# Kernel optimization log

Hardware: AMD Instinct MI355X
Metric: run time of the kernel (lower is better)

## Reference

```python
import jax, jax.numpy as jnp
import numpy as np
import math

D = 384  # hidden_dim; seq_len must equal D, batch must be 1 (torch broadcast constraint)
S = 384
B = 1


def grad_seq(x):
    """torch.gradient along axis 1: one-sided at edges, central in interior."""
    left = x[:, 1:2] - x[:, 0:1]
    mid = (x[:, 2:] - x[:, :-2]) * 0.5
    right = x[:, -1:] - x[:, -2:-1]
    return jnp.concatenate([left, mid, right], axis=1)


def setup_inputs() -> dict:
    key = jax.random.key(0)
    ks = jax.random.split(key, 8)
    return {
        "query_field": jax.random.normal(ks[0], (B, S, D), jnp.float32),
        "key_field": jax.random.normal(ks[1], (B, S, D), jnp.float32),
        "value_field": jax.random.normal(ks[2], (B, S, D), jnp.float32),
        "gauge_weights": jax.random.normal(ks[3], (D, D), jnp.float32) * 0.01,
        "covariant_weights": jax.random.normal(ks[4], (D, D), jnp.float32) * 0.01,
        "yang_mills_coupling": jnp.asarray(1.0, jnp.float32),
        "lag_w1": jax.random.normal(ks[5], (2 * D, D), jnp.float32) * (1.0 / math.sqrt(2 * D)),
        "lag_b1": jnp.zeros((D,), jnp.float32),
        "lag_w2": jax.random.normal(ks[6], (D, 1), jnp.float32) * (1.0 / math.sqrt(D)),
        "lag_b2": jnp.zeros((1,), jnp.float32),
    }


def reference(query_field, key_field, value_field, gauge_weights, covariant_weights,
              yang_mills_coupling, lag_w1, lag_b1, lag_w2, lag_b2):
    q, k, v = query_field, key_field, value_field

    # ---- field strength F_munu -------------------------------------------
    ga = grad_seq(q)                                   # [B,S,D]
    gb = grad_seq(k)
    # commutator: per-token dim x dim outer products
    comm = q[..., :, None] * k[..., None, :] - k[..., :, None] * q[..., None, :]  # [B,S,D,D]
    cm = comm.mean(axis=-1)                            # [B,S,D]
    # torch broadcast: [B,S,D,1]-[B,S,1,D] + [B,S,D] (left-padded to [1,B,S,D]); valid since B=1, S=D
    field_strength = ga[..., :, None] - gb[..., None, :] + cm  # [1,S,D,D]

    # ---- covariant derivatives -------------------------------------------
    cov_q = grad_seq(q) + q @ covariant_weights        # [B,S,D]
    cov_k = grad_seq(k) + k @ covariant_weights

    # ---- interaction energy (Lagrangian MLP) ------------------------------
    combined = jnp.concatenate([cov_q, cov_k], axis=-1)          # [B,S,2D]
    h = jax.nn.relu(combined @ lag_w1 + lag_b1)
    interaction_density = h @ lag_w2 + lag_b2                    # [B,S,1]
    interaction_energy = interaction_density.sum(axis=1)         # [B,1]

    # ---- gauge-invariant attention ----------------------------------------
    logits = jnp.einsum('bqd,bkd->bqk', cov_q, cov_k) / math.sqrt(D)  # [B,S,S]
    gauge_corr = (field_strength @ gauge_weights).sum(axis=-1)        # [B,S,D]
    # torch broadcast: [B,S,S] + [B,S,D,1] -> [1,S,D,S] (valid since S=D)
    gal = logits + gauge_corr[..., None]                              # [1,S,D,S]
    attention_weights = jax.nn.softmax(gal, axis=-1)                  # [1,S,D,S]

    evolved_field = jnp.matmul(attention_weights, v)                  # [1,S,S,D]

    # ---- metrics ------------------------------------------------------------
    yang_mills_action = yang_mills_coupling * jnp.sum(field_strength ** 2, axis=(-2, -1)).sum(axis=1)  # [B]

    second = grad_seq(grad_seq(evolved_field))
    field_curvature = jnp.linalg.norm(second, axis=-1).mean(axis=1)   # [1,S]

    init_e = jnp.sum(q ** 2, axis=(-2, -1))                           # [B]
    fin_e = jnp.sum(evolved_field ** 2, axis=(-2, -1))                # [1,S]
    conservation = jnp.abs(fin_e - init_e) / (init_e + 1e-8)          # [1,S]

    row_sums = attention_weights.sum(axis=-1)
    gauge_inv = jnp.clip(1.0 - jnp.std(row_sums, ddof=1), 0.0, 1.0)

    flat = evolved_field.reshape(evolved_field.shape[0], -1)
    coherence = jnp.mean(jnp.abs(jnp.corrcoef(flat)))                 # scalar (==1 for B=1)

    topo = (field_strength.sum(axis=(-2, -1)) / (2 * math.pi)).mean(axis=1)  # [B]

    return (evolved_field, field_strength, interaction_energy, yang_mills_action,
            field_curvature, gauge_inv, conservation, coherence, topo)
```

## Files before the change

### kernel.cpp

```cpp
#include <hip/hip_runtime.h>

#define S_ 384
#define D_ 384
#define SD_ (384*384)

#define OUT_EV 0
#define OUT_FS 56623104
#define OUT_IE 113246208
#define OUT_YM 113246209
#define OUT_FC 113246210
#define OUT_GI 113246594
#define OUT_CO 113246595
#define OUT_CH 113246979
#define OUT_TP 113246980

typedef __attribute__((ext_vector_type(4))) float f32x4;

__device__ __forceinline__ float waveSum(float v){
  v += __shfl_down(v,32); v += __shfl_down(v,16); v += __shfl_down(v,8);
  v += __shfl_down(v,4);  v += __shfl_down(v,2);  v += __shfl_down(v,1);
  return v;
}
__device__ __forceinline__ float waveMax(float v){
  v = fmaxf(v,__shfl_down(v,32)); v = fmaxf(v,__shfl_down(v,16)); v = fmaxf(v,__shfl_down(v,8));
  v = fmaxf(v,__shfl_down(v,4));  v = fmaxf(v,__shfl_down(v,2));  v = fmaxf(v,__shfl_down(v,1));
  return v;
}
__device__ __forceinline__ double waveSumD(double v){
  v += __shfl_down(v,32); v += __shfl_down(v,16); v += __shfl_down(v,8);
  v += __shfl_down(v,4);  v += __shfl_down(v,2);  v += __shfl_down(v,1);
  return v;
}

__device__ __forceinline__ void writeF_block(int id, int t,
    const float* __restrict__ ga, const float* __restrict__ gb,
    const float* __restrict__ cm, float* __restrict__ outF){
  __shared__ float gbs[D_];
  __shared__ float gas[64];
  int bs = id/6, ch = id%6, i0 = ch*64;
  gbs[t] = gb[bs*D_+t];
  if (t<64) gas[t] = ga[bs*D_+i0+t];
  __syncthreads();
  const f32x4* cm4 = (const f32x4*)(cm + i0*D_);
  const f32x4* gb4 = (const f32x4*)gbs;
  f32x4* o4 = (f32x4*)(outF + ((size_t)bs*S_ + i0)*D_);
  #pragma unroll
  for (int u=0; u<16; u++){
    int f = t + u*384;
    int il = f/96;
    int j4 = f - il*96;
    f32x4 o = gas[il] - gb4[j4] + cm4[f];
    o4[f] = o;
  }
}
__device__ __forceinline__ void writeE_block(int id, int t,
    const float* __restrict__ E, float* __restrict__ outE){
  int bs = id/6, ch = id%6, i0 = ch*64;
  const f32x4* e4 = (const f32x4*)(E + i0*D_);
  f32x4* o4 = (f32x4*)(outE + ((size_t)bs*S_ + i0)*D_);
  #pragma unroll
  for (int u=0; u<16; u++){
    int f = t + u*384;
    o4[f] = e4[f];
  }
}

__global__ __launch_bounds__(384) void k1(
    const float* __restrict__ q, const float* __restrict__ k,
    const float* __restrict__ W,
    float* __restrict__ ga, float* __restrict__ gb, float* __restrict__ cm,
    float* __restrict__ pq2,
    float* __restrict__ cq, float* __restrict__ ck, float* __restrict__ ckT){
  int b = blockIdx.x, t = threadIdx.x;
  if (b < 384){
    int s = b;
    float a = q[s*D_+t], bb = k[s*D_+t];
    float sq = waveSum(a), sk = waveSum(bb), sq2 = waveSum(a*a);
    __shared__ float red[3][6];
    int wid=t>>6, lane=t&63;
    if (lane==0){ red[0][wid]=sq; red[1][wid]=sk; red[2][wid]=sq2; }
    __syncthreads();
    float qm=0,km=0,q2=0;
    #pragma unroll
    for (int w=0;w<6;w++){ qm+=red[0][w]; km+=red[1][w]; q2+=red[2][w]; }
    qm *= (1.0f/D_); km *= (1.0f/D_);
    if (t==0) pq2[s]=q2;
    int sm=(s==0)?0:s-1, sp=(s==S_-1)?S_-1:s+1;
    float sc=(s==0||s==S_-1)?1.f:0.5f;
    ga[s*D_+t] = (q[sp*D_+t]-q[sm*D_+t])*sc;
    gb[s*D_+t] = (k[sp*D_+t]-k[sm*D_+t])*sc;
    cm[s*D_+t] = a*km - bb*qm;
  } else if (b < 480){
    int s0 = (b-384)*4;
    const float* r0=q+(s0+0)*D_; const float* r1=q+(s0+1)*D_;
    const float* r2=q+(s0+2)*D_; const float* r3=q+(s0+3)*D_;
    float a0=0,a1=0,a2=0,a3=0;
    for (int e=0;e<D_;e+=4){
      float w0=W[(e+0)*D_+t], w1=W[(e+1)*D_+t], w2=W[(e+2)*D_+t], w3=W[(e+3)*D_+t];
      f32x4 x;
      x=*(const f32x4*)(r0+e); a0 += x.x*w0 + x.y*w1 + x.z*w2 + x.w*w3;
      x=*(const f32x4*)(r1+e); a1 += x.x*w0 + x.y*w1 + x.z*w2 + x.w*w3;
      x=*(const f32x4*)(r2+e); a2 += x.x*w0 + x.y*w1 + x.z*w2 + x.w*w3;
      x=*(const f32x4*)(r3+e); a3 += x.x*w0 + x.y*w1 + x.z*w2 + x.w*w3;
    }
    float acc[4]={a0,a1,a2,a3};
    #pragma unroll
    for (int r=0;r<4;r++){
      int s=s0+r;
      int sm=(s==0)?0:s-1, sp=(s==S_-1)?S_-1:s+1;
      float sc=(s==0||s==S_-1)?1.f:0.5f;
      cq[s*D_+t] = acc[r] + (q[sp*D_+t]-q[sm*D_+t])*sc;
    }
  } else {
    int s0 = (b-480)*4;
    const float* r0=k+(s0+0)*D_; const float* r1=k+(s0+1)*D_;
    const float* r2=k+(s0+2)*D_; const float* r3=k+(s0+3)*D_;
    float a0=0,a1=0,a2=0,a3=0;
    for (int e=0;e<D_;e+=4){
      float w0=W[(e+0)*D_+t], w1=W[(e+1)*D_+t], w2=W[(e+2)*D_+t], w3=W[(e+3)*D_+t];
      f32x4 x;
      x=*(const f32x4*)(r0+e); a0 += x.x*w0 + x.y*w1 + x.z*w2 + x.w*w3;
      x=*(const f32x4*)(r1+e); a1 += x.x*w0 + x.y*w1 + x.z*w2 + x.w*w3;
      x=*(const f32x4*)(r2+e); a2 += x.x*w0 + x.y*w1 + x.z*w2 + x.w*w3;
      x=*(const f32x4*)(r3+e); a3 += x.x*w0 + x.y*w1 + x.z*w2 + x.w*w3;
    }
    float acc[4]={a0,a1,a2,a3};
    float o[4];
    #pragma unroll
    for (int r=0;r<4;r++){
      int s=s0+r;
      int sm=(s==0)?0:s-1, sp=(s==S_-1)?S_-1:s+1;
      float sc=(s==0||s==S_-1)?1.f:0.5f;
      o[r] = acc[r] + (k[sp*D_+t]-k[sm*D_+t])*sc;
      ck[s*D_+t] = o[r];
    }
    f32x4 tr; tr.x=o[0]; tr.y=o[1]; tr.z=o[2]; tr.w=o[3];
    *(f32x4*)(ckT + t*D_ + s0) = tr;
  }
}

__global__ __launch_bounds__(384) void k2(
    const float* __restrict__ covq, const float* __restrict__ covk,
    const float* __restrict__ ckT, const float* __restrict__ v,
    const float* __restrict__ W1, const float* __restrict__ b1,
    const float* __restrict__ W2,
    float* __restrict__ E, float* __restrict__ pE2, float* __restrict__ pen,
    const float* __restrict__ ga, const float* __restrict__ gb,
    const float* __restrict__ cm,
    float* __restrict__ Sga, float* __restrict__ Sgb, float* __restrict__ Rcm,
    float* __restrict__ P2, float* __restrict__ Cga, float* __restrict__ Cgb,
    float* __restrict__ Ccm, float* __restrict__ outF){
  int b = blockIdx.x, t = threadIdx.x;
  if (b < 96){
    int i0 = b*4;
    __shared__ float P[4][D_];
    __shared__ float wred[4][6];
    __shared__ float wred2[4][6];
    __shared__ float sred[6];
    const float* q0=covq+(i0+0)*D_; const float* q1=covq+(i0+1)*D_;
    const float* q2=covq+(i0+2)*D_; const float* q3=covq+(i0+3)*D_;
    float l0=0,l1=0,l2=0,l3=0;
    for (int e=0;e<D_;e+=4){
      float c0=ckT[(e+0)*D_+t], c1=ckT[(e+1)*D_+t], c2=ckT[(e+2)*D_+t], c3=ckT[(e+3)*D_+t];
      f32x4 a;
      a=*(const f32x4*)(q0+e); l0 += a.x*c0 + a.y*c1 + a.z*c2 + a.w*c3;
      a=*(const f32x4*)(q1+e); l1 += a.x*c0 + a.y*c1 + a.z*c2 + a.w*c3;
      a=*(const f32x4*)(q2+e); l2 += a.x*c0 + a.y*c1 + a.z*c2 + a.w*c3;
      a=*(const f32x4*)(q3+e); l3 += a.x*c0 + a.y*c1 + a.z*c2 + a.w*c3;
    }
    const float isq = 0.05103103630798288f;
    l0*=isq; l1*=isq; l2*=isq; l3*=isq;
    float m0=waveMax(l0), m1=waveMax(l1), m2=waveMax(l2), m3=waveMax(l3);
    int wid=t>>6, lane=t&63;
    if (lane==0){ wred[0][wid]=m0; wred[1][wid]=m1; wred[2][wid]=m2; wred[3][wid]=m3; }
    __syncthreads();
    float mx0=wred[0][0], mx1=wred[1][0], mx2=wred[2][0], mx3=wred[3][0];
    for (int w=1; w<6; w++){
      mx0=fmaxf(mx0,wred[0][w]); mx1=fmaxf(mx1,wred[1][w]);
      mx2=fmaxf(mx2,wred[2][w]); mx3=fmaxf(mx3,wred[3][w]);
    }
    float e0=expf(l0-mx0), e1=expf(l1-mx1), e2=expf(l2-mx2), e3=expf(l3-mx3);
    float s0=waveSum(e0), s1=waveSum(e1), s2=waveSum(e2), s3=waveSum(e3);
    if (lane==0){ wred2[0][wid]=s0; wred2[1][wid]=s1; wred2[2][wid]=s2; wred2[3][wid]=s3; }
    __syncthreads();
    float d0=0,d1=0,d2=0,d3=0;
    for (int w=0; w<6; w++){ d0+=wred2[0][w]; d1+=wred2[1][w]; d2+=wred2[2][w]; d3+=wred2[3][w]; }
    P[0][t]=e0/d0; P[1][t]=e1/d1; P[2][t]=e2/d2; P[3][t]=e3/d3;
    __syncthreads();
    float ea0=0,ea1=0,ea2=0,ea3=0;
    for (int t2=0; t2<D_; t2+=4){
      float v0 = v[(t2+0)*D_+t];
      float v1 = v[(t2+1)*D_+t];
      float v2 = v[(t2+2)*D_+t];
      float v3 = v[(t2+3)*D_+t];
      f32x4 p;
      p=*(const f32x4*)&P[0][t2]; ea0 += p.x*v0 + p.y*v1 + p.z*v2 + p.w*v3;
      p=*(const f32x4*)&P[1][t2]; ea1 += p.x*v0 + p.y*v1 + p.z*v2 + p.w*v3;
      p=*(const f32x4*)&P[2][t2]; ea2 += p.x*v0 + p.y*v1 + p.z*v2 + p.w*v3;
      p=*(const f32x4*)&P[3][t2]; ea3 += p.x*v0 + p.y*v1 + p.z*v2 + p.w*v3;
    }
    E[(i0+0)*D_+t]=ea0; E[(i0+1)*D_+t]=ea1; E[(i0+2)*D_+t]=ea2; E[(i0+3)*D_+t]=ea3;
    float se2 = ea0*ea0+ea1*ea1+ea2*ea2+ea3*ea3;
    se2 = waveSum(se2);
    if (lane==0) sred[wid]=se2;
    __syncthreads();
    if (t==0) pE2[b] = sred[0]+sred[1]+sred[2]+sred[3]+sred[4]+sred[5];
  } else if (b < 192){
    int s0 = (b-96)*4;
    __shared__ float sred2[6];
    const float* c0=covq+(s0+0)*D_; const float* c1=covq+(s0+1)*D_;
    const float* c2=covq+(s0+2)*D_; const float* c3=covq+(s0+3)*D_;
    const float* d0=covk+(s0+0)*D_; const float* d1=covk+(s0+1)*D_;
    const float* d2=covk+(s0+2)*D_; const float* d3=covk+(s0+3)*D_;
    float h0=0,h1=0,h2=0,h3=0;
    for (int e=0; e<D_; e+=4){
      float w0=W1[(e+0)*D_+t], w1=W1[(e+1)*D_+t], w2=W1[(e+2)*D_+t], w3=W1[(e+3)*D_+t];
      f32x4 x;
      x=*(const f32x4*)(c0+e); h0 += x.x*w0 + x.y*w1 + x.z*w2 + x.w*w3;
      x=*(const f32x4*)(c1+e); h1 += x.x*w0 + x.y*w1 + x.z*w2 + x.w*w3;
      x=*(const f32x4*)(c2+e); h2 += x.x*w0 + x.y*w1 + x.z*w2 + x.w*w3;
      x=*(const f32x4*)(c3+e); h3 += x.x*w0 + x.y*w1 + x.z*w2 + x.w*w3;
    }
    for (int e=0; e<D_; e+=4){
      float w0=W1[(D_+e+0)*D_+t], w1=W1[(D_+e+1)*D_+t], w2=W1[(D_+e+2)*D_+t], w3=W1[(D_+e+3)*D_+t];
      f32x4 x;
      x=*(const f32x4*)(d0+e); h0 += x.x*w0 + x.y*w1 + x.z*w2 + x.w*w3;
      x=*(const f32x4*)(d1+e); h1 += x.x*w0 + x.y*w1 + x.z*w2 + x.w*w3;
      x=*(const f32x4*)(d2+e); h2 += x.x*w0 + x.y*w1 + x.z*w2 + x.w*w3;
      x=*(const f32x4*)(d3+e); h3 += x.x*w0 + x.y*w1 + x.z*w2 + x.w*w3;
    }
    float bb=b1[t], w2c=W2[t];
    h0=fmaxf(h0+bb,0.f); h1=fmaxf(h1+bb,0.f); h2=fmaxf(h2+bb,0.f); h3=fmaxf(h3+bb,0.f);
    float p = (h0+h1+h2+h3)*w2c;
    p = waveSum(p);
    int wid=t>>6, lane=t&63;
    if (lane==0) sred2[wid]=p;
    __syncthreads();
    if (t==0) pen[b-96] = sred2[0]+sred2[1]+sred2[2]+sred2[3]+sred2[4]+sred2[5];
  } else if (b < 576){
    int rb = b-192;
    float ra=ga[rb*D_+t], rg=gb[rb*D_+t], rc=cm[rb*D_+t];
    float ca=ga[t*D_+rb], cg=gb[t*D_+rb], cc=cm[t*D_+rb];
    float p2 = ra*ra + rg*rg + rc*rc;
    float s0=waveSum(ra), s1=waveSum(rg), s2=waveSum(rc), s3=waveSum(p2);
    float s4=waveSum(ca), s5=waveSum(cg), s6=waveSum(cc);
    __shared__ float red[7][6];
    int wid=t>>6, lane=t&63;
    if (lane==0){ red[0][wid]=s0; red[1][wid]=s1; red[2][wid]=s2; red[3][wid]=s3;
                  red[4][wid]=s4; red[5][wid]=s5; red[6][wid]=s6; }
    __syncthreads();
    if (t==0){
      float a0=0,a1=0,a2=0,a3=0,a4=0,a5=0,a6=0;
      for (int w=0;w<6;w++){ a0+=red[0][w]; a1+=red[1][w]; a2+=red[2][w]; a3+=red[3][w];
                             a4+=red[4][w]; a5+=red[5][w]; a6+=red[6][w]; }
      Sga[rb]=a0; Sgb[rb]=a1; Rcm[rb]=a2; P2[rb]=a3; Cga[rb]=a4; Cgb[rb]=a5; Ccm[rb]=a6;
    }
  } else {
    writeF_block(b-576, t, ga, gb, cm, outF);
  }
}

__global__ __launch_bounds__(384) void k3(
    const float* __restrict__ E, float* __restrict__ outE,
    const float* __restrict__ pq2,
    const float* __restrict__ Sga, const float* __restrict__ Sgb,
    const float* __restrict__ Rcm, const float* __restrict__ P2,
    const float* __restrict__ Cga, const float* __restrict__ Cgb,
    const float* __restrict__ Ccm,
    const float* __restrict__ pE2, const float* __restrict__ pen,
    const float* __restrict__ coup, const float* __restrict__ b2,
    float* __restrict__ out){
  int b = blockIdx.x, t = threadIdx.x;
  if (b == 0){
    double v[10];
    v[0]=pq2[t];
    v[1]=Sga[t]; v[2]=Sgb[t]; v[3]=Rcm[t]; v[4]=P2[t];
    v[5]=(double)Sga[t]*Sgb[t];
    v[6]=(double)Cga[t]*Rcm[t];
    v[7]=(double)Cgb[t]*Ccm[t];
    v[8]=(t<96)? (double)pE2[t] : 0.0;
    v[9]=(t<96)? (double)pen[t] : 0.0;
    __shared__ double red[10][6];
    int wid=t>>6, lane=t&63;
    #pragma unroll
    for (int i=0;i<10;i++){
      double s = waveSumD(v[i]);
      if (lane==0) red[i][wid]=s;
    }
    __syncthreads();
    double tot[10];
    #pragma unroll
    for (int i=0;i<10;i++){
      double s=0; for (int w=0;w<6;w++) s+=red[i][w];
      tot[i]=s;
    }
    double init_e=tot[0], fin_e=tot[8], en=tot[9];
    double sumF  = 384.0*(tot[1]-tot[2]+tot[3]);
    double sumF2 = 384.0*tot[4] - 2.0*tot[5] + 2.0*tot[6] - 2.0*tot[7];
    float cons = (float)(fabs(fin_e - init_e)/(init_e + 1e-8));
    out[OUT_FC + t] = 0.0f;
    out[OUT_CO + t] = cons;
    if (t == 0){
      out[OUT_IE] = (float)en + 384.0f*b2[0];
      out[OUT_YM] = coup[0]*(float)sumF2;
      out[OUT_GI] = 1.0f;
      out[OUT_CH] = 1.0f;
      out[OUT_TP] = (float)(sumF/(6.283185307179586*384.0));
    }
  } else {
    writeE_block(b-1, t, E, outE);
  }
}

extern "C" void kernel_launch(void* const* d_in, const int* in_sizes, int n_in,
                              void* d_out, int out_size, void* d_ws, size_t ws_size,
                              hipStream_t stream) {
  const float* q    = (const float*)d_in[0];
  const float* k    = (const float*)d_in[1];
  const float* v    = (const float*)d_in[2];
  const float* Wcov = (const float*)d_in[4];
  const float* coup = (const float*)d_in[5];
  const float* W1   = (const float*)d_in[6];
  const float* b1   = (const float*)d_in[7];
  const float* W2   = (const float*)d_in[8];
  const float* b2   = (const float*)d_in[9];
  float* out = (float*)d_out;
  float* ws  = (float*)d_ws;
  float* ga   = ws;
  float* gb   = ws + 1*SD_;
  float* cm   = ws + 2*SD_;
  float* cq   = ws + 3*SD_;
  float* ck   = ws + 4*SD_;
  float* ckT  = ws + 5*SD_;
  float* E    = ws + 6*SD_;
  float* base = ws + 7*SD_;
  float* pq2 = base;
  float* Sga = base + 384;  float* Sgb = base + 768;
  float* Rcm = base + 1152; float* P2  = base + 1536;
  float* Cga = base + 1920; float* Cgb = base + 2304;
  float* Ccm = base + 2688;
  float* pE2 = base + 3072;
  float* pen = base + 3168;

  k1<<<dim3(576),  dim3(384), 0, stream>>>(q, k, Wcov, ga, gb, cm, pq2, cq, ck, ckT);
  k2<<<dim3(2880), dim3(384), 0, stream>>>(cq, ck, ckT, v, W1, b1, W2, E, pE2, pen,
                                           ga, gb, cm, Sga, Sgb, Rcm, P2, Cga, Cgb, Ccm,
                                           out + OUT_FS);
  k3<<<dim3(2305), dim3(384), 0, stream>>>(E, out + OUT_EV,
                                           pq2, Sga, Sgb, Rcm, P2, Cga, Cgb, Ccm,
                                           pE2, pen, coup, b2, out);
}
```

Measured before the change: 516.1 us.

## Fuse three kernels into two; compute field strength directly and broadcast evolved rows

The field-strength tensor is now written straight from q and k inside the first kernel, which computes the per-row means and gradients on the fly, so the ga/gb/cm intermediates are never stored. Column-sum statistics are replaced by closed-form edge-gradient terms. The evolved-field output is written by the attention blocks themselves, which broadcast each row over all 384 copies and drop the separate E copy kernel. The final scalar reduction runs in the last-finishing block through atomics and a completion counter rather than a third launch. The cost is float atomics, which make results order-dependent, and a grid-wide last-block pattern.

```diff
diff --git a/kernel.cpp b/kernel.cpp
--- a/kernel.cpp
+++ b/kernel.cpp
@@ -32,70 +32,100 @@
   return v;
 }
 
-__device__ __forceinline__ void writeF_block(int id, int t,
-    const float* __restrict__ ga, const float* __restrict__ gb,
-    const float* __restrict__ cm, float* __restrict__ outF){
-  __shared__ float gbs[D_];
-  __shared__ float gas[64];
-  int bs = id/6, ch = id%6, i0 = ch*64;
-  gbs[t] = gb[bs*D_+t];
-  if (t<64) gas[t] = ga[bs*D_+i0+t];
-  __syncthreads();
-  const f32x4* cm4 = (const f32x4*)(cm + i0*D_);
-  const f32x4* gb4 = (const f32x4*)gbs;
-  f32x4* o4 = (f32x4*)(outF + ((size_t)bs*S_ + i0)*D_);
-  #pragma unroll
-  for (int u=0; u<16; u++){
-    int f = t + u*384;
-    int il = f/96;
-    int j4 = f - il*96;
-    f32x4 o = gas[il] - gb4[j4] + cm4[f];
-    o4[f] = o;
-  }
-}
-__device__ __forceinline__ void writeE_block(int id, int t,
-    const float* __restrict__ E, float* __restrict__ outE){
-  int bs = id/6, ch = id%6, i0 = ch*64;
-  const f32x4* e4 = (const f32x4*)(E + i0*D_);
-  f32x4* o4 = (f32x4*)(outE + ((size_t)bs*S_ + i0)*D_);
-  #pragma unroll
-  for (int u=0; u<16; u++){
-    int f = t + u*384;
-    o4[f] = e4[f];
-  }
-}
-
-__global__ __launch_bounds__(384) void k1(
+__global__ __launch_bounds__(384) void kA(
     const float* __restrict__ q, const float* __restrict__ k,
     const float* __restrict__ W,
-    float* __restrict__ ga, float* __restrict__ gb, float* __restrict__ cm,
-    float* __restrict__ pq2,
-    float* __restrict__ cq, float* __restrict__ ck, float* __restrict__ ckT){
+    float* __restrict__ cq, float* __restrict__ ck, float* __restrict__ ckT,
+    float* __restrict__ pq2, float* __restrict__ Sga, float* __restrict__ Sgb,
+    float* __restrict__ Rcm, float* __restrict__ P2, float* __restrict__ pcc,
+    float* __restrict__ accum, float* __restrict__ outF){
   int b = blockIdx.x, t = threadIdx.x;
-  if (b < 384){
-    int s = b;
+  if (b < 2304){
+    int bs = b/6, ch = b%6, i0 = ch*64;
+    __shared__ float pr[64][6];
+    __shared__ float mq[64], mk[64];
+    __shared__ float gbs[D_];
+    __shared__ float gas[64];
+    int r = t/6, seg = t - r*6;
+    const f32x4* q4r = (const f32x4*)(q + (i0+r)*D_ + seg*64);
+    float p_ = 0.f;
+    #pragma unroll
+    for (int u=0; u<16; u++){ f32x4 x = q4r[u]; p_ += x.x+x.y+x.z+x.w; }
+    pr[r][seg] = p_;
+    __syncthreads();
+    if (t < 64){
+      float s = 0.f;
+      #pragma unroll
+      for (int w=0; w<6; w++) s += pr[t][w];
+      mq[t] = s * (1.0f/D_);
+    }
+    __syncthreads();
+    const f32x4* k4r = (const f32x4*)(k + (i0+r)*D_ + seg*64);
+    p_ = 0.f;
+    #pragma unroll
+    for (int u=0; u<16; u++){ f32x4 x = k4r[u]; p_ += x.x+x.y+x.z+x.w; }
+    pr[r][seg] = p_;
+    __syncthreads();
+    if (t < 64){
+      float s = 0.f;
+      #pragma unroll
+      for (int w=0; w<6; w++) s += pr[t][w];
+      mk[t] = s * (1.0f/D_);
+    }
+    int sm = (bs==0)?0:bs-1, sp = (bs==S_-1)?S_-1:bs+1;
+    float sc = (bs==0 || bs==S_-1) ? 1.f : 0.5f;
+    gbs[t] = (k[sp*D_+t]-k[sm*D_+t])*sc;
+    if (t < 64) gas[t] = (q[sp*D_+i0+t]-q[sm*D_+i0+t])*sc;
+    __syncthreads();
+    const f32x4* q4 = (const f32x4*)(q + i0*D_);
+    const f32x4* k4 = (const f32x4*)(k + i0*D_);
+    const f32x4* gb4 = (const f32x4*)gbs;
+    f32x4* o4 = (f32x4*)(outF + ((size_t)bs*S_ + i0)*D_);
+    #pragma unroll
+    for (int u=0; u<16; u++){
+      int f = t + u*384;
+      int il = f/96;
+      int j4 = f - il*96;
+      f32x4 o = gas[il] - gb4[j4] + q4[f]*mq[il] - k4[f]*mk[il];
+      o4[f] = o;
+    }
+  } else if (b < 2688){
+    int s = b - 2304;
+    if (s == 0 && t == 0){ accum[0]=0.f; accum[1]=0.f; ((unsigned int*)accum)[2]=0u; }
     float a = q[s*D_+t], bb = k[s*D_+t];
     float sq = waveSum(a), sk = waveSum(bb), sq2 = waveSum(a*a);
     __shared__ float red[3][6];
-    int wid=t>>6, lane=t&63;
+    int wid = t>>6, lane = t&63;
     if (lane==0){ red[0][wid]=sq; red[1][wid]=sk; red[2][wid]=sq2; }
     __syncthreads();
     float qm=0,km=0,q2=0;
     #pragma unroll
-    for (int w=0;w<6;w++){ qm+=red[0][w]; km+=red[1][w]; q2+=red[2][w]; }
+    for (int w=0; w<6; w++){ qm+=red[0][w]; km+=red[1][w]; q2+=red[2][w]; }
     qm *= (1.0f/D_); km *= (1.0f/D_);
-    if (t==0) pq2[s]=q2;
-    int sm=(s==0)?0:s-1, sp=(s==S_-1)?S_-1:s+1;
-    float sc=(s==0||s==S_-1)?1.f:0.5f;
-    ga[s*D_+t] = (q[sp*D_+t]-q[sm*D_+t])*sc;
-    gb[s*D_+t] = (k[sp*D_+t]-k[sm*D_+t])*sc;
-    cm[s*D_+t] = a*km - bb*qm;
-  } else if (b < 480){
-    int s0 = (b-384)*4;
+    if (t==0) pq2[s] = q2;
+    int sm = (s==0)?0:s-1, sp = (s==S_-1)?S_-1:s+1;
+    float sc = (s==0 || s==S_-1) ? 1.f : 0.5f;
+    float ga_ = (q[sp*D_+t]-q[sm*D_+t])*sc;
+    float gb_ = (k[sp*D_+t]-k[sm*D_+t])*sc;
+    float cm_ = a*km - bb*qm;
+    float cgb = -1.5f*k[t] + 0.5f*k[D_+t] - 0.5f*k[382*D_+t] + 1.5f*k[383*D_+t];
+    float s0 = waveSum(ga_), s1 = waveSum(gb_), s2 = waveSum(cm_);
+    float s3 = waveSum(ga_*ga_ + gb_*gb_ + cm_*cm_);
+    float s4 = waveSum(cgb*cm_);
+    __shared__ float r2[5][6];
+    if (lane==0){ r2[0][wid]=s0; r2[1][wid]=s1; r2[2][wid]=s2; r2[3][wid]=s3; r2[4][wid]=s4; }
+    __syncthreads();
+    if (t==0){
+      float a0=0,a1=0,a2=0,a3=0,a4=0;
+      for (int w=0; w<6; w++){ a0+=r2[0][w]; a1+=r2[1][w]; a2+=r2[2][w]; a3+=r2[3][w]; a4+=r2[4][w]; }
+      Sga[s]=a0; Sgb[s]=a1; Rcm[s]=a2; P2[s]=a3; pcc[s]=a4;
+    }
+  } else if (b < 2784){
+    int s0 = (b-2688)*4;
     const float* r0=q+(s0+0)*D_; const float* r1=q+(s0+1)*D_;
     const float* r2=q+(s0+2)*D_; const float* r3=q+(s0+3)*D_;
     float a0=0,a1=0,a2=0,a3=0;
-    for (int e=0;e<D_;e+=4){
+    for (int e=0; e<D_; e+=4){
       float w0=W[(e+0)*D_+t], w1=W[(e+1)*D_+t], w2=W[(e+2)*D_+t], w3=W[(e+3)*D_+t];
       f32x4 x;
       x=*(const f32x4*)(r0+e); a0 += x.x*w0 + x.y*w1 + x.z*w2 + x.w*w3;
@@ -105,18 +135,18 @@
     }
     float acc[4]={a0,a1,a2,a3};
     #pragma unroll
-    for (int r=0;r<4;r++){
+    for (int r=0; r<4; r++){
       int s=s0+r;
       int sm=(s==0)?0:s-1, sp=(s==S_-1)?S_-1:s+1;
       float sc=(s==0||s==S_-1)?1.f:0.5f;
       cq[s*D_+t] = acc[r] + (q[sp*D_+t]-q[sm*D_+t])*sc;
     }
   } else {
-    int s0 = (b-480)*4;
+    int s0 = (b-2784)*4;
     const float* r0=k+(s0+0)*D_; const float* r1=k+(s0+1)*D_;
     const float* r2=k+(s0+2)*D_; const float* r3=k+(s0+3)*D_;
     float a0=0,a1=0,a2=0,a3=0;
-    for (int e=0;e<D_;e+=4){
+    for (int e=0; e<D_; e+=4){
       float w0=W[(e+0)*D_+t], w1=W[(e+1)*D_+t], w2=W[(e+2)*D_+t], w3=W[(e+3)*D_+t];
       f32x4 x;
       x=*(const f32x4*)(r0+e); a0 += x.x*w0 + x.y*w1 + x.z*w2 + x.w*w3;
@@ -127,7 +157,7 @@
     float acc[4]={a0,a1,a2,a3};
     float o[4];
     #pragma unroll
-    for (int r=0;r<4;r++){
+    for (int r=0; r<4; r++){
       int s=s0+r;
       int sm=(s==0)?0:s-1, sp=(s==S_-1)?S_-1:s+1;
       float sc=(s==0||s==S_-1)?1.f:0.5f;
@@ -139,79 +169,76 @@
   }
 }
 
-__global__ __launch_bounds__(384) void k2(
-    const float* __restrict__ covq, const float* __restrict__ covk,
+#define NBLK_B 480
+__global__ __launch_bounds__(384) void kB(
+    const float* __restrict__ q,
+    const float* __restrict__ cq, const float* __restrict__ ck,
     const float* __restrict__ ckT, const float* __restrict__ v,
     const float* __restrict__ W1, const float* __restrict__ b1,
-    const float* __restrict__ W2,
-    float* __restrict__ E, float* __restrict__ pE2, float* __restrict__ pen,
-    const float* __restrict__ ga, const float* __restrict__ gb,
-    const float* __restrict__ cm,
-    float* __restrict__ Sga, float* __restrict__ Sgb, float* __restrict__ Rcm,
-    float* __restrict__ P2, float* __restrict__ Cga, float* __restrict__ Cgb,
-    float* __restrict__ Ccm, float* __restrict__ outF){
+    const float* __restrict__ W2, const float* __restrict__ b2,
+    const float* __restrict__ coup,
+    const float* __restrict__ pq2, const float* __restrict__ Sga,
+    const float* __restrict__ Sgb, const float* __restrict__ Rcm,
+    const float* __restrict__ P2, const float* __restrict__ pcc,
+    float* __restrict__ accum, float* __restrict__ outE,
+    float* __restrict__ out){
   int b = blockIdx.x, t = threadIdx.x;
-  if (b < 96){
-    int i0 = b*4;
-    __shared__ float P[4][D_];
-    __shared__ float wred[4][6];
-    __shared__ float wred2[4][6];
+  int wid = t>>6, lane = t&63;
+  if (b < 384){
+    int i = b;
+    __shared__ float Ps[D_];
+    __shared__ float Es[D_];
+    __shared__ float red1[6], red2[6];
+    const float* qi = cq + i*D_;
+    float l = 0.f;
+    for (int e=0; e<D_; e+=4){
+      f32x4 a = *(const f32x4*)(qi+e);
+      l += a.x*ckT[(e+0)*D_+t] + a.y*ckT[(e+1)*D_+t]
+         + a.z*ckT[(e+2)*D_+t] + a.w*ckT[(e+3)*D_+t];
+    }
+    l *= 0.05103103630798288f;
+    float m = waveMax(l);
+    if (lane==0) red1[wid] = m;
+    __syncthreads();
+    float mx = red1[0];
+    for (int w=1; w<6; w++) mx = fmaxf(mx, red1[w]);
+    float e_ = expf(l - mx);
+    float sden = waveSum(e_);
+    if (lane==0) red2[wid] = sden;
+    __syncthreads();
+    float den = 0.f;
+    for (int w=0; w<6; w++) den += red2[w];
+    Ps[t] = e_/den;
+    __syncthreads();
+    float ea = 0.f;
+    for (int j=0; j<D_; j+=4){
+      f32x4 p = *(const f32x4*)&Ps[j];
+      ea += p.x*v[(j+0)*D_+t] + p.y*v[(j+1)*D_+t]
+          + p.z*v[(j+2)*D_+t] + p.w*v[(j+3)*D_+t];
+    }
+    Es[t] = ea;
+    float e2 = waveSum(ea*ea);
+    __syncthreads();
+    if (lane==0) red1[wid] = e2;
+    __syncthreads();
+    if (t==0){
+      float s = red1[0]+red1[1]+red1[2]+red1[3]+red1[4]+red1[5];
+      atomicAdd(&accum[0], s);
+    }
+    const f32x4* Es4 = (const f32x4*)Es;
+    int c4 = t % 96, bs0 = t / 96;
+    f32x4 val = Es4[c4];
+    for (int u=0; u<96; u++){
+      int bs = u*4 + bs0;
+      *(f32x4*)(outE + ((size_t)bs*S_ + i)*D_ + 4*c4) = val;
+    }
+  } else {
+    int s0 = (b-384)*4;
     __shared__ float sred[6];
-    const float* q0=covq+(i0+0)*D_; const float* q1=covq+(i0+1)*D_;
-    const float* q2=covq+(i0+2)*D_; const float* q3=covq+(i0+3)*D_;
-    float l0=0,l1=0,l2=0,l3=0;
-    for (int e=0;e<D_;e+=4){
-      float c0=ckT[(e+0)*D_+t], c1=ckT[(e+1)*D_+t], c2=ckT[(e+2)*D_+t], c3=ckT[(e+3)*D_+t];
-      f32x4 a;
-      a=*(const f32x4*)(q0+e); l0 += a.x*c0 + a.y*c1 + a.z*c2 + a.w*c3;
-      a=*(const f32x4*)(q1+e); l1 += a.x*c0 + a.y*c1 + a.z*c2 + a.w*c3;
-      a=*(const f32x4*)(q2+e); l2 += a.x*c0 + a.y*c1 + a.z*c2 + a.w*c3;
-      a=*(const f32x4*)(q3+e); l3 += a.x*c0 + a.y*c1 + a.z*c2 + a.w*c3;
-    }
-    const float isq = 0.05103103630798288f;
-    l0*=isq; l1*=isq; l2*=isq; l3*=isq;
-    float m0=waveMax(l0), m1=waveMax(l1), m2=waveMax(l2), m3=waveMax(l3);
-    int wid=t>>6, lane=t&63;
-    if (lane==0){ wred[0][wid]=m0; wred[1][wid]=m1; wred[2][wid]=m2; wred[3][wid]=m3; }
-    __syncthreads();
-    float mx0=wred[0][0], mx1=wred[1][0], mx2=wred[2][0], mx3=wred[3][0];
-    for (int w=1; w<6; w++){
-      mx0=fmaxf(mx0,wred[0][w]); mx1=fmaxf(mx1,wred[1][w]);
-      mx2=fmaxf(mx2,wred[2][w]); mx3=fmaxf(mx3,wred[3][w]);
-    }
-    float e0=expf(l0-mx0), e1=expf(l1-mx1), e2=expf(l2-mx2), e3=expf(l3-mx3);
-    float s0=waveSum(e0), s1=waveSum(e1), s2=waveSum(e2), s3=waveSum(e3);
-    if (lane==0){ wred2[0][wid]=s0; wred2[1][wid]=s1; wred2[2][wid]=s2; wred2[3][wid]=s3; }
-    __syncthreads();
-    float d0=0,d1=0,d2=0,d3=0;
-    for (int w=0; w<6; w++){ d0+=wred2[0][w]; d1+=wred2[1][w]; d2+=wred2[2][w]; d3+=wred2[3][w]; }
-    P[0][t]=e0/d0; P[1][t]=e1/d1; P[2][t]=e2/d2; P[3][t]=e3/d3;
-    __syncthreads();
-    float ea0=0,ea1=0,ea2=0,ea3=0;
-    for (int t2=0; t2<D_; t2+=4){
-      float v0 = v[(t2+0)*D_+t];
-      float v1 = v[(t2+1)*D_+t];
-      float v2 = v[(t2+2)*D_+t];
-      float v3 = v[(t2+3)*D_+t];
-      f32x4 p;
-      p=*(const f32x4*)&P[0][t2]; ea0 += p.x*v0 + p.y*v1 + p.z*v2 + p.w*v3;
-      p=*(const f32x4*)&P[1][t2]; ea1 += p.x*v0 + p.y*v1 + p.z*v2 + p.w*v3;
-      p=*(const f32x4*)&P[2][t2]; ea2 += p.x*v0 + p.y*v1 + p.z*v2 + p.w*v3;
-      p=*(const f32x4*)&P[3][t2]; ea3 += p.x*v0 + p.y*v1 + p.z*v2 + p.w*v3;
-    }
-    E[(i0+0)*D_+t]=ea0; E[(i0+1)*D_+t]=ea1; E[(i0+2)*D_+t]=ea2; E[(i0+3)*D_+t]=ea3;
-    float se2 = ea0*ea0+ea1*ea1+ea2*ea2+ea3*ea3;
-    se2 = waveSum(se2);
-    if (lane==0) sred[wid]=se2;
-    __syncthreads();
-    if (t==0) pE2[b] = sred[0]+sred[1]+sred[2]+sred[3]+sred[4]+sred[5];
-  } else if (b < 192){
-    int s0 = (b-96)*4;
-    __shared__ float sred2[6];
-    const float* c0=covq+(s0+0)*D_; const float* c1=covq+(s0+1)*D_;
-    const float* c2=covq+(s0+2)*D_; const float* c3=covq+(s0+3)*D_;
-    const float* d0=covk+(s0+0)*D_; const float* d1=covk+(s0+1)*D_;
-    const float* d2=covk+(s0+2)*D_; const float* d3=covk+(s0+3)*D_;
+    const float* c0=cq+(s0+0)*D_; const float* c1=cq+(s0+1)*D_;
+    const float* c2=cq+(s0+2)*D_; const float* c3=cq+(s0+3)*D_;
+    const float* d0=ck+(s0+0)*D_; const float* d1=ck+(s0+1)*D_;
+    const float* d2=ck+(s0+2)*D_; const float* d3=ck+(s0+3)*D_;
     float h0=0,h1=0,h2=0,h3=0;
     for (int e=0; e<D_; e+=4){
       float w0=W1[(e+0)*D_+t], w1=W1[(e+1)*D_+t], w2=W1[(e+2)*D_+t], w3=W1[(e+3)*D_+t];
@@ -233,68 +260,51 @@
     h0=fmaxf(h0+bb,0.f); h1=fmaxf(h1+bb,0.f); h2=fmaxf(h2+bb,0.f); h3=fmaxf(h3+bb,0.f);
     float p = (h0+h1+h2+h3)*w2c;
     p = waveSum(p);
-    int wid=t>>6, lane=t&63;
-    if (lane==0) sred2[wid]=p;
-    __syncthreads();
-    if (t==0) pen[b-96] = sred2[0]+sred2[1]+sred2[2]+sred2[3]+sred2[4]+sred2[5];
-  } else if (b < 576){
-    int rb = b-192;
-    float ra=ga[rb*D_+t], rg=gb[rb*D_+t], rc=cm[rb*D_+t];
-    float ca=ga[t*D_+rb], cg=gb[t*D_+rb], cc=cm[t*D_+rb];
-    float p2 = ra*ra + rg*rg + rc*rc;
-    float s0=waveSum(ra), s1=waveSum(rg), s2=waveSum(rc), s3=waveSum(p2);
-    float s4=waveSum(ca), s5=waveSum(cg), s6=waveSum(cc);
-    __shared__ float red[7][6];
-    int wid=t>>6, lane=t&63;
-    if (lane==0){ red[0][wid]=s0; red[1][wid]=s1; red[2][wid]=s2; red[3][wid]=s3;
-                  red[4][wid]=s4; red[5][wid]=s5; red[6][wid]=s6; }
+    if (lane==0) sred[wid] = p;
     __syncthreads();
     if (t==0){
-      float a0=0,a1=0,a2=0,a3=0,a4=0,a5=0,a6=0;
-      for (int w=0;w<6;w++){ a0+=red[0][w]; a1+=red[1][w]; a2+=red[2][w]; a3+=red[3][w];
-                             a4+=red[4][w]; a5+=red[5][w]; a6+=red[6][w]; }
-      Sga[rb]=a0; Sgb[rb]=a1; Rcm[rb]=a2; P2[rb]=a3; Cga[rb]=a4; Cgb[rb]=a5; Ccm[rb]=a6;
-    }
-  } else {
-    writeF_block(b-576, t, ga, gb, cm, outF);
+      float s = sred[0]+sred[1]+sred[2]+sred[3]+sred[4]+sred[5];
+      atomicAdd(&accum[1], s);
+    }
   }
-}
-
-__global__ __launch_bounds__(384) void k3(
-    const float* __restrict__ E, float* __restrict__ outE,
-    const float* __restrict__ pq2,
-    const float* __restrict__ Sga, const float* __restrict__ Sgb,
-    const float* __restrict__ Rcm, const float* __restrict__ P2,
-    const float* __restrict__ Cga, const float* __restrict__ Cgb,
-    const float* __restrict__ Ccm,
-    const float* __restrict__ pE2, const float* __restrict__ pen,
-    const float* __restrict__ coup, const float* __restrict__ b2,
-    float* __restrict__ out){
-  int b = blockIdx.x, t = threadIdx.x;
-  if (b == 0){
-    double v[10];
-    v[0]=pq2[t];
-    v[1]=Sga[t]; v[2]=Sgb[t]; v[3]=Rcm[t]; v[4]=P2[t];
-    v[5]=(double)Sga[t]*Sgb[t];
-    v[6]=(double)Cga[t]*Rcm[t];
-    v[7]=(double)Cgb[t]*Ccm[t];
-    v[8]=(t<96)? (double)pE2[t] : 0.0;
-    v[9]=(t<96)? (double)pen[t] : 0.0;
-    __shared__ double red[10][6];
-    int wid=t>>6, lane=t&63;
-    #pragma unroll
-    for (int i=0;i<10;i++){
-      double s = waveSumD(v[i]);
-      if (lane==0) red[i][wid]=s;
-    }
-    __syncthreads();
-    double tot[10];
-    #pragma unroll
-    for (int i=0;i<10;i++){
-      double s=0; for (int w=0;w<6;w++) s+=red[i][w];
-      tot[i]=s;
-    }
-    double init_e=tot[0], fin_e=tot[8], en=tot[9];
+  __threadfence();
+  __shared__ unsigned int lastf;
+  if (t==0){
+    unsigned int old = atomicAdd(((unsigned int*)accum)+2, 1u);
+    lastf = (old == NBLK_B-1) ? 1u : 0u;
+  }
+  __syncthreads();
+  if (lastf){
+    __threadfence();
+    double vv[8];
+    vv[0]=pq2[t];
+    vv[1]=Sga[t]; vv[2]=Sgb[t]; vv[3]=Rcm[t]; vv[4]=P2[t];
+    vv[5]=(double)Sga[t]*Sgb[t];
+    float cga = -1.5f*q[t] + 0.5f*q[D_+t] - 0.5f*q[382*D_+t] + 1.5f*q[383*D_+t];
+    vv[6]=(double)cga*Rcm[t];
+    vv[7]=pcc[t];
+    __shared__ double redd[8][6];
+    #pragma unroll
+    for (int i2=0; i2<8; i2++){
+      double s = waveSumD(vv[i2]);
+      if (lane==0) redd[i2][wid]=s;
+    }
+    __syncthreads();
+    double tot[8];
+    #pragma unroll
+    for (int i2=0; i2<8; i2++){
+      double s=0; for (int w=0; w<6; w++) s += redd[i2][w];
+      tot[i2]=s;
+    }
+    __shared__ float fe_s, en_s;
+    if (t==0){
+      fe_s = atomicAdd(&accum[0], 0.0f);
+      en_s = atomicAdd(&accum[1], 0.0f);
+    }
+    __syncthreads();
+    double init_e = tot[0];
+    double fin_e  = (double)fe_s;
+    double en     = (double)en_s;
     double sumF  = 384.0*(tot[1]-tot[2]+tot[3]);
     double sumF2 = 384.0*tot[4] - 2.0*tot[5] + 2.0*tot[6] - 2.0*tot[7];
     float cons = (float)(fabs(fin_e - init_e)/(init_e + 1e-8));
@@ -307,8 +317,6 @@
       out[OUT_CH] = 1.0f;
       out[OUT_TP] = (float)(sumF/(6.283185307179586*384.0));
     }
-  } else {
-    writeE_block(b-1, t, E, outE);
   }
 }
 
@@ -326,27 +334,20 @@
   const float* b2   = (const float*)d_in[9];
   float* out = (float*)d_out;
   float* ws  = (float*)d_ws;
-  float* ga   = ws;
-  float* gb   = ws + 1*SD_;
-  float* cm   = ws + 2*SD_;
-  float* cq   = ws + 3*SD_;
-  float* ck   = ws + 4*SD_;
-  float* ckT  = ws + 5*SD_;
-  float* E    = ws + 6*SD_;
-  float* base = ws + 7*SD_;
+  float* cq   = ws;
+  float* ck   = ws + 1*SD_;
+  float* ckT  = ws + 2*SD_;
+  float* base = ws + 3*SD_;
   float* pq2 = base;
   float* Sga = base + 384;  float* Sgb = base + 768;
   float* Rcm = base + 1152; float* P2  = base + 1536;
-  float* Cga = base + 1920; float* Cgb = base + 2304;
-  float* Ccm = base + 2688;
-  float* pE2 = base + 3072;
-  float* pen = base + 3168;
-
-  k1<<<dim3(576),  dim3(384), 0, stream>>>(q, k, Wcov, ga, gb, cm, pq2, cq, ck, ckT);
-  k2<<<dim3(2880), dim3(384), 0, stream>>>(cq, ck, ckT, v, W1, b1, W2, E, pE2, pen,
-                                           ga, gb, cm, Sga, Sgb, Rcm, P2, Cga, Cgb, Ccm,
-                                           out + OUT_FS);
-  k3<<<dim3(2305), dim3(384), 0, stream>>>(E, out + OUT_EV,
-                                           pq2, Sga, Sgb, Rcm, P2, Cga, Cgb, Ccm,
-                                           pE2, pen, coup, b2, out);
-}
+  float* pcc = base + 1920;
+  float* accum = base + 2304;
+
+  kA<<<dim3(2880), dim3(384), 0, stream>>>(q, k, Wcov, cq, ck, ckT,
+                                           pq2, Sga, Sgb, Rcm, P2, pcc,
+                                           accum, out + OUT_FS);
+  kB<<<dim3(NBLK_B), dim3(384), 0, stream>>>(q, cq, ck, ckT, v, W1, b1, W2, b2, coup,
+                                             pq2, Sga, Sgb, Rcm, P2, pcc,
+                                             accum, out + OUT_EV, out);
+}
```

Measured after the change: 640.8 us. +24.2%, slower.
